# Optimization experiments

Hardware: AMD Instinct MI355X
Metric: run time of the kernel (lower is better)

## Reference

```python
import jax, jax.numpy as jnp
import numpy as np

NP_ = 20000   # paper nodes
NA_ = 20000   # author nodes
E_AP = 400000
E_PP = 400000
D_IN, D_H, HEADS, D_HEAD, D_FF, D_OUT = 128, 256, 8, 32, 2048, 64


def setup_inputs() -> dict:
    key = jax.random.key(0)
    ks = iter(jax.random.split(key, 48))
    def nrm(shape, s=0.1):
        return jax.random.normal(next(ks), shape, jnp.float32) * s
    inp = {
        'feat_paper': nrm((NP_, D_IN), 1.0),
        'feat_author': nrm((NA_, D_IN), 1.0),
        'W_in_p': nrm((D_H, D_IN)), 'b_in_p': nrm((D_H,), 0.05),
        'W_in_a': nrm((D_H, D_IN)), 'b_in_a': nrm((D_H,), 0.05),
        'W_gat_ap': nrm((D_H, D_H)), 'al_ap': nrm((HEADS, D_HEAD)), 'ar_ap': nrm((HEADS, D_HEAD)), 'b_gat_ap': nrm((D_H,), 0.05),
        'W_gat_pp': nrm((D_H, D_H)), 'al_pp': nrm((HEADS, D_HEAD)), 'ar_pp': nrm((HEADS, D_HEAD)), 'b_gat_pp': nrm((D_H,), 0.05),
        'Wqkv_s': nrm((3 * D_H, D_H)), 'bqkv_s': nrm((3 * D_H,), 0.05), 'Wo_s': nrm((D_H, D_H)), 'bo_s': nrm((D_H,), 0.05),
        'Wqkv_c': nrm((3 * D_H, D_H)), 'bqkv_c': nrm((3 * D_H,), 0.05), 'Wo_c': nrm((D_H, D_H)), 'bo_c': nrm((D_H,), 0.05),
        'W_ff1': nrm((D_FF, D_H)), 'b_ff1': nrm((D_FF,), 0.05),
        'W_ff2': nrm((D_H, D_FF)), 'b_ff2': nrm((D_H,), 0.05),
        'ln1_g': jnp.ones((D_H,), jnp.float32), 'ln1_b': jnp.zeros((D_H,), jnp.float32),
        'ln2_g': jnp.ones((D_H,), jnp.float32), 'ln2_b': jnp.zeros((D_H,), jnp.float32),
        'ln3_g': jnp.ones((D_H,), jnp.float32), 'ln3_b': jnp.zeros((D_H,), jnp.float32),
        'W_pred': nrm((D_OUT, 3 * D_H)), 'b_pred': nrm((D_OUT,), 0.05),
        'ap_src': jax.random.randint(next(ks), (E_AP,), 0, NA_),
        'ap_dst': jax.random.randint(next(ks), (E_AP,), 0, NP_),
        'pp_src': jax.random.randint(next(ks), (E_PP,), 0, NP_),
        'pp_dst': jax.random.randint(next(ks), (E_PP,), 0, NP_),
    }
    return inp


def _leaky(x):
    return jnp.where(x > 0, x, 0.2 * x)  # DGL GATConv negative_slope=0.2


def _gat(x, src, dst, W, al, ar, b):
    """DGL GATConv on homogeneous graph with self-loops appended (eval mode)."""
    N = x.shape[0]
    h = (x @ W.T).reshape(N, HEADS, D_HEAD)          # fc has no bias in GATConv
    el = (h * al[None]).sum(-1)                      # (N, H)
    er = (h * ar[None]).sum(-1)                      # (N, H)
    sl = jnp.arange(N, dtype=src.dtype)              # self loops (add_self_loop)
    s = jnp.concatenate([src, sl])
    d = jnp.concatenate([dst, sl])
    e = _leaky(el[s] + er[d])                        # (E+N, H)
    m = jax.ops.segment_max(e, d, num_segments=N)    # edge-softmax per dst
    a = jnp.exp(e - m[d])
    z = jax.ops.segment_sum(a, d, num_segments=N)
    out = jax.ops.segment_sum(a[:, :, None] * h[s], d, num_segments=N)
    out = out / z[:, :, None] + b.reshape(1, HEADS, D_HEAD)
    return out.reshape(N, D_H)                       # flatten(start_dim=1)


def _ln(x, g, b):
    mu = x.mean(-1, keepdims=True)
    v = ((x - mu) ** 2).mean(-1, keepdims=True)
    return (x - mu) / jnp.sqrt(v + 1e-5) * g + b


def _mha(xq, xkv, Wqkv, bqkv, Wo, bo):
    Wq, Wk, Wv = jnp.split(Wqkv, 3, axis=0)
    bq, bk, bv = jnp.split(bqkv, 3)
    B, S, _ = xq.shape
    Sk = xkv.shape[1]
    q = (xq @ Wq.T + bq).reshape(B, S, HEADS, D_HEAD)
    k = (xkv @ Wk.T + bk).reshape(B, Sk, HEADS, D_HEAD)
    v = (xkv @ Wv.T + bv).reshape(B, Sk, HEADS, D_HEAD)
    att = jnp.einsum('bqhd,bkhd->bhqk', q, k) * (D_HEAD ** -0.5)
    a = jax.nn.softmax(att, axis=-1)
    o = jnp.einsum('bhqk,bkhd->bqhd', a, v).reshape(B, S, D_H)
    return o @ Wo.T + bo


def reference(feat_paper, feat_author, W_in_p, b_in_p, W_in_a, b_in_a,
              W_gat_ap, al_ap, ar_ap, b_gat_ap, W_gat_pp, al_pp, ar_pp, b_gat_pp,
              Wqkv_s, bqkv_s, Wo_s, bo_s, Wqkv_c, bqkv_c, Wo_c, bo_c,
              W_ff1, b_ff1, W_ff2, b_ff2, ln1_g, ln1_b, ln2_g, ln2_b, ln3_g, ln3_b,
              W_pred, b_pred, ap_src, ap_dst, pp_src, pp_dst):
    # fc_in per node type
    hp = feat_paper @ W_in_p.T + b_in_p              # (NP, D_H)
    ha = feat_author @ W_in_a.T + b_in_a             # (NA, D_H)
    Na = ha.shape[0]
    # etype 'ap': bipartite author->paper, to_homogeneous orders [author; paper]
    x_ap = jnp.concatenate([ha, hp], axis=0)
    out_ap = _gat(x_ap, ap_src, ap_dst + Na, W_gat_ap, al_ap, ar_ap, b_gat_ap)[Na:]
    # etype 'pp': paper->paper (single node set)
    out_pp = _gat(hp, pp_src, pp_dst, W_gat_pp, al_pp, ar_pp, b_gat_pp)
    # h dict order: 'paper', 'paper-author', 'paper-paper'
    tgt = jnp.stack([hp, out_ap, out_pp], axis=1)    # (NP, 3, D_H)
    # TransformerDecoderLayer (post-norm, relu, eval): memory = tgt
    x = _ln(tgt + _mha(tgt, tgt, Wqkv_s, bqkv_s, Wo_s, bo_s), ln1_g, ln1_b)
    x = _ln(x + _mha(x, tgt, Wqkv_c, bqkv_c, Wo_c, bo_c), ln2_g, ln2_b)
    ff = jax.nn.relu(x @ W_ff1.T + b_ff1) @ W_ff2.T + b_ff2
    z = _ln(x + ff, ln3_g, ln3_b)
    return z.reshape(z.shape[0], -1) @ W_pred.T + b_pred
```

## Files before the change

kernel.cpp:

```cpp
#include <hip/hip_runtime.h>
#include <hip/hip_bf16.h>
#include <cstdint>
#include <cstddef>

#define NP_N 20000
#define NA_N 20000
#define E_AP_N 400000
#define E_PP_N 400000

typedef __attribute__((ext_vector_type(8))) short bf16x8;
typedef __attribute__((ext_vector_type(4))) float f32x4;

__device__ __forceinline__ float b2f(ushort u) { return __uint_as_float(((uint32_t)u) << 16); }
__device__ __forceinline__ ushort f2b(float f) {
    uint32_t x = __float_as_uint(f);
    return (ushort)((x + 0x7fffu + ((x >> 16) & 1u)) >> 16);
}

#define LGKM_BARRIER() do { \
    asm volatile("s_waitcnt lgkmcnt(0)" ::: "memory"); \
    __builtin_amdgcn_s_barrier(); \
    __builtin_amdgcn_sched_barrier(0); \
} while (0)

#define NJOBS 14
struct PackJobs {
    const float* src[NJOBS];
    void* dst[NJOBS];
    int M[NJOBS], K[NJOBS];
    int type[NJOBS];
    int nquad[NJOBS];
    int blk0[NJOBS];
};

__global__ void pack_all_kernel(PackJobs J)
{
    int b = blockIdx.x;
    int j = 0;
    while (j + 1 < NJOBS && b >= J.blk0[j + 1]) ++j;
    int u = (b - J.blk0[j]) * 256 + threadIdx.x;
    if (u >= J.nquad[j]) return;
    int ty = J.type[j];
    const float* src = J.src[j];
    if (ty == 3) {
        float4 v = ((const float4*)src)[u];
        ushort4 o;
        o.x = f2b(v.x); o.y = f2b(v.y); o.z = f2b(v.z); o.w = f2b(v.w);
        ((ushort4*)J.dst[j])[u] = o;
    } else if (ty == 4) {
        int4 z = {0, 0, 0, 0};
        ((int4*)J.dst[j])[u] = z;
    } else if (ty == 0) {
        int M = J.M[j], K = J.K[j];
        int KT = K >> 5;
        int q = u & 1023;
        int jt = u >> 10;
        int t = jt % KT, jj = jt / KT;
        int ks = q >> 8, rem = q & 255;
        int r = rem >> 1;
        int e0 = (rem & 1) * 4;
        int row = jj * 128 + r;
        ushort4 o = {0, 0, 0, 0};
        if (row < M) {
            const float* s = src + (size_t)row * K + t * 32 + ks * 8 + e0;
            o.x = f2b(s[0]); o.y = f2b(s[1]); o.z = f2b(s[2]); o.w = f2b(s[3]);
        }
        ((ushort4*)J.dst[j])[u] = o;
    } else if (ty == 1) {
        int q = u & 2047, chunk = u >> 11;
        int s = q >> 6, rem = q & 63;
        int fl = rem >> 1, e0 = (rem & 1) * 4;
        const float* sp = src + (size_t)(chunk * 32 + fl) * 256 + s * 8 + e0;
        ushort4 o;
        o.x = f2b(sp[0]); o.y = f2b(sp[1]); o.z = f2b(sp[2]); o.w = f2b(sp[3]);
        ((ushort4*)J.dst[j])[u] = o;
    } else {
        int q = u & 2047, chunk = u >> 11;
        int s2 = q >> 9, rem = q & 511;
        int c = rem >> 1, e0 = (rem & 1) * 4;
        const float* sp = src + (size_t)c * 2048 + chunk * 32 + s2 * 8 + e0;
        ushort4 o;
        o.x = f2b(sp[0]); o.y = f2b(sp[1]); o.z = f2b(sp[2]); o.w = f2b(sp[3]);
        ((ushort4*)J.dst[j])[u] = o;
    }
}

template <int OUT_MODE>
__global__ __launch_bounds__(256) void gemm_mfma(
    const ushort* __restrict__ A, const ushort* __restrict__ Bp,
    const float* __restrict__ bias, void* __restrict__ Cv,
    int N, int M, int K, int lda)
{
    __shared__ __align__(16) ushort Ab[3][4096];
    __shared__ __align__(16) ushort Bb[3][4096];
    const int tid = threadIdx.x;
    const int lane = tid & 63;
    const int w = tid >> 6;
    const int wr = w >> 1, wc = w & 1;
    const int row0 = blockIdx.x * 128;
    const int col0 = blockIdx.y * 128;
    const int KT = K >> 5;
    const ushort* Bbase = Bp + (size_t)blockIdx.y * KT * 4096;
    f32x4 acc[4][4] = {};

    size_t aoff[2];
#pragma unroll
    for (int i = 0; i < 2; ++i) {
        int r = row0 + i * 64 + lane;
        if (r > N - 1) r = N - 1;
        aoff[i] = (size_t)r * lda + w * 8;
    }

    auto stage = [&](int buf, int t) {
        const int k0 = t << 5;
#pragma unroll
        for (int i = 0; i < 2; ++i) {
            __builtin_amdgcn_global_load_lds(
                (const __attribute__((address_space(1))) void*)(A + aoff[i] + k0),
                (__attribute__((address_space(3))) void*)(&Ab[buf][(w * 2 + i) * 512]), 16, 0, 0);
        }
#pragma unroll
        for (int i = 0; i < 2; ++i) {
            __builtin_amdgcn_global_load_lds(
                (const __attribute__((address_space(1))) void*)(Bbase + (size_t)t * 4096 + (w * 2 + i) * 512 + lane * 8),
                (__attribute__((address_space(3))) void*)(&Bb[buf][(w * 2 + i) * 512]), 16, 0, 0);
        }
    };

    stage(0, 0);
    stage(1, 1);

    int cur = 0;
    for (int t = 0; t < KT; ++t) {
        if (t + 1 < KT) { asm volatile("s_waitcnt vmcnt(4)" ::: "memory"); }
        else            { asm volatile("s_waitcnt vmcnt(0)" ::: "memory"); }
        __builtin_amdgcn_s_barrier();
        __builtin_amdgcn_sched_barrier(0);
        if (t + 2 < KT) {
            int nb = cur - 1; if (nb < 0) nb = 2;
            stage(nb, t + 2);
        }

        bf16x8 af[4], bfr[4];
        const int ks = lane >> 4;
        const int rl = lane & 15;
#pragma unroll
        for (int m = 0; m < 4; ++m)
            af[m] = *(const bf16x8*)&Ab[cur][ks * 1024 + (wr * 64 + m * 16 + rl) * 8];
#pragma unroll
        for (int n = 0; n < 4; ++n)
            bfr[n] = *(const bf16x8*)&Bb[cur][ks * 1024 + (wc * 64 + n * 16 + rl) * 8];
#pragma unroll
        for (int m = 0; m < 4; ++m)
#pragma unroll
            for (int n = 0; n < 4; ++n)
                acc[m][n] = __builtin_amdgcn_mfma_f32_16x16x32_bf16(af[m], bfr[n], acc[m][n], 0, 0, 0);

        cur = (cur == 2) ? 0 : cur + 1;
    }

#pragma unroll
    for (int m = 0; m < 4; ++m) {
#pragma unroll
        for (int n = 0; n < 4; ++n) {
            int gc = col0 + wc * 64 + n * 16 + (lane & 15);
            if (gc >= M) continue;
            float bv = bias ? bias[gc] : 0.f;
#pragma unroll
            for (int r = 0; r < 4; ++r) {
                int grow = row0 + wr * 64 + m * 16 + (lane >> 4) * 4 + r;
                if (grow >= N) continue;
                float v = acc[m][n][r] + bv;
                if (OUT_MODE == 2) v = fmaxf(v, 0.f);
                if (OUT_MODE == 1) ((float*)Cv)[(size_t)grow * M + gc] = v;
                else ((ushort*)Cv)[(size_t)grow * M + gc] = f2b(v);
            }
        }
    }
}

static inline void gemm_bf(const ushort* A, const ushort* Bp, const float* bias, void* C,
                           int N, int M, int K, int lda, int mode, hipStream_t s)
{
    dim3 g((N + 127) / 128, (M + 127) / 128);
    if (mode == 0)      gemm_mfma<0><<<g, 256, 0, s>>>(A, Bp, bias, C, N, M, K, lda);
    else if (mode == 1) gemm_mfma<1><<<g, 256, 0, s>>>(A, Bp, bias, C, N, M, K, lda);
    else                gemm_mfma<2><<<g, 256, 0, s>>>(A, Bp, bias, C, N, M, K, lda);
}

__global__ __launch_bounds__(512) void ff_fused_kernel(
    const ushort* __restrict__ X, const ushort* __restrict__ W1p,
    const ushort* __restrict__ W2p, const float* __restrict__ b1,
    const float* __restrict__ b2, ushort* __restrict__ ffout, int N)
{
    __shared__ __align__(16) ushort W1buf[2][8192];
    __shared__ __align__(16) ushort W2buf[2][8192];
    __shared__ __align__(16) ushort Sbuf[4096];
    const int tid = threadIdx.x;
    const int lane = tid & 63;
    const int w = tid >> 6;
    const int wr = w >> 1, wc = w & 1;
    const int row0 = blockIdx.x * 128;
    const int rl = lane & 15;
    const int ks = lane >> 4;

    bf16x8 xf[2][8];
#pragma unroll
    for (int m = 0; m < 2; ++m) {
        int gr = row0 + wr * 32 + m * 16 + rl;
        if (gr > N - 1) gr = N - 1;
        const ushort* xrow = X + (size_t)gr * 256 + ks * 8;
#pragma unroll
        for (int kc = 0; kc < 8; ++kc)
            xf[m][kc] = *(const bf16x8*)(xrow + kc * 32);
    }

    f32x4 oacc[2][8] = {};

    auto stage = [&](int buf, int fc) {
#pragma unroll
        for (int i = 0; i < 4; ++i) {
            int ii = w * 4 + i;
            const ushort* src;
            ushort* dst;
            if (ii < 16) {
                src = W1p + (size_t)fc * 8192 + ii * 512 + lane * 8;
                dst = &W1buf[buf][ii * 512];
            } else {
                src = W2p + (size_t)fc * 8192 + (ii - 16) * 512 + lane * 8;
                dst = &W2buf[buf][(ii - 16) * 512];
            }
            __builtin_amdgcn_global_load_lds(
                (const __attribute__((address_space(1))) void*)src,
                (__attribute__((address_space(3))) void*)dst, 16, 0, 0);
        }
    };

    stage(0, 0);

    for (int fc = 0; fc < 64; ++fc) {
        const int cur = fc & 1;
        asm volatile("s_waitcnt vmcnt(0)" ::: "memory");
        __builtin_amdgcn_s_barrier();
        __builtin_amdgcn_sched_barrier(0);
        if (fc + 1 < 64) stage(cur ^ 1, fc + 1);

        f32x4 sacc[2] = {};
#pragma unroll
        for (int kc = 0; kc < 8; ++kc) {
            bf16x8 w1f = *(const bf16x8*)&W1buf[cur][(kc * 4 + ks) * 256 + (wc * 16 + rl) * 8];
#pragma unroll
            for (int m = 0; m < 2; ++m)
                sacc[m] = __builtin_amdgcn_mfma_f32_16x16x32_bf16(w1f, xf[m][kc], sacc[m], 0, 0, 0);
        }
        {
            const int f0 = fc * 32;
            const int fb = wc * 16 + ks * 4;
            const int sidx = wc * 2 + (ks >> 1);
            const int e0 = (ks & 1) * 4;
            float4 b1v = *(const float4*)&b1[f0 + fb];
#pragma unroll
            for (int m = 0; m < 2; ++m) {
                ushort4 o;
                o.x = f2b(fmaxf(sacc[m][0] + b1v.x, 0.f));
                o.y = f2b(fmaxf(sacc[m][1] + b1v.y, 0.f));
                o.z = f2b(fmaxf(sacc[m][2] + b1v.z, 0.f));
                o.w = f2b(fmaxf(sacc[m][3] + b1v.w, 0.f));
                *(ushort4*)&Sbuf[(sidx * 128 + wr * 32 + m * 16 + rl) * 8 + e0] = o;
            }
        }
        LGKM_BARRIER();

        {
            bf16x8 sf[2];
#pragma unroll
            for (int m = 0; m < 2; ++m)
                sf[m] = *(const bf16x8*)&Sbuf[(ks * 128 + wr * 32 + m * 16 + rl) * 8];
#pragma unroll
            for (int n = 0; n < 8; ++n) {
                bf16x8 w2f = *(const bf16x8*)&W2buf[cur][ks * 2048 + (wc * 128 + n * 16 + rl) * 8];
#pragma unroll
                for (int m = 0; m < 2; ++m)
                    oacc[m][n] = __builtin_amdgcn_mfma_f32_16x16x32_bf16(sf[m], w2f, oacc[m][n], 0, 0, 0);
            }
        }
    }

#pragma unroll
    for (int n = 0; n < 8; ++n) {
        int c = wc * 128 + n * 16 + rl;
        float bv = b2[c];
#pragma unroll
        for (int m = 0; m < 2; ++m) {
            int rbase = row0 + wr * 32 + m * 16 + ks * 4;
#pragma unroll
            for (int r = 0; r < 4; ++r) {
                int gr = rbase + r;
                if (gr < N) ffout[(size_t)gr * 256 + c] = f2b(oacc[m][n][r] + bv);
            }
        }
    }
}

__global__ void copy_col0_kernel(const ushort* __restrict__ src, ushort* __restrict__ tgt, int n)
{
    int i = blockIdx.x * blockDim.x + threadIdx.x;
    if (i >= n) return;
    int p = i >> 6, c = i & 63;
    ((ushort4*)tgt)[(size_t)p * 192 + c] = ((const ushort4*)src)[(size_t)p * 64 + c];
}

__global__ void attn_lr_all_kernel(
    const ushort* __restrict__ h0, const float* __restrict__ al0, const float* __restrict__ ar0,
    float* __restrict__ el0, float* __restrict__ er0,
    const ushort* __restrict__ h1, const float* __restrict__ al1, const float* __restrict__ ar1,
    float* __restrict__ el1, float* __restrict__ er1)
{
    int idx = blockIdx.x * blockDim.x + threadIdx.x;
    if (idx >= 480000) return;
    const ushort* h; const float *a1, *a2; float *el, *er; int i;
    if (idx < 320000) { h = h0; a1 = al0; a2 = ar0; el = el0; er = er0; i = idx; }
    else { h = h1; a1 = al1; a2 = ar1; el = el1; er = er1; i = idx - 320000; }
    int hd = i & 7;
    const ushort* hp = h + (size_t)(i >> 3) * 256 + hd * 32;
    const float* p1 = a1 + hd * 32;
    const float* p2 = a2 + hd * 32;
    float s1 = 0.f, s2 = 0.f;
#pragma unroll
    for (int j = 0; j < 8; ++j) {
        ushort4 t = ((const ushort4*)hp)[j];
        float v0 = b2f(t.x), v1 = b2f(t.y), v2 = b2f(t.z), v3 = b2f(t.w);
        s1 = fmaf(v0, p1[j * 4 + 0], s1); s2 = fmaf(v0, p2[j * 4 + 0], s2);
        s1 = fmaf(v1, p1[j * 4 + 1], s1); s2 = fmaf(v1, p2[j * 4 + 1], s2);
        s1 = fmaf(v2, p1[j * 4 + 2], s1); s2 = fmaf(v2, p2[j * 4 + 2], s2);
        s1 = fmaf(v3, p1[j * 4 + 3], s1); s2 = fmaf(v3, p2[j * 4 + 3], s2);
    }
    el[i] = s1;
    er[i] = s2;
}

__global__ void count2_kernel(const int* __restrict__ d0, int* __restrict__ c0,
                              const int* __restrict__ d1, int* __restrict__ c1, int E)
{
    int e = blockIdx.x * blockDim.x + threadIdx.x;
    if (e < E) atomicAdd(&c0[d0[e]], 1);
    else if (e < 2 * E) atomicAdd(&c1[d1[e - E]], 1);
}

__global__ void exscan2_kernel(int* __restrict__ deg0, int* __restrict__ offs0,
                               int* __restrict__ deg1, int* __restrict__ offs1, int N)
{
    int* deg = blockIdx.x ? deg1 : deg0;
    int* offs = blockIdx.x ? offs1 : offs0;
    __shared__ int sbuf[1024];
    __shared__ int carry;
    int tid = threadIdx.x;
    if (tid == 0) carry = 0;
    __syncthreads();
    for (int base = 0; base < N; base += 1024) {
        int i = base + tid;
        int v = (i < N) ? deg[i] : 0;
        sbuf[tid] = v;
        __syncthreads();
        for (int off = 1; off < 1024; off <<= 1) {
            int t = (tid >= off) ? sbuf[tid - off] : 0;
            __syncthreads();
            sbuf[tid] += t;
            __syncthreads();
        }
        if (i < N) offs[i] = carry + sbuf[tid] - v;
        int chunk_total = sbuf[1023];
        __syncthreads();
        if (tid == 0) carry += chunk_total;
        __syncthreads();
    }
    if (tid == 0) offs[N] = carry;
    __syncthreads();
    for (int i = tid; i < N; i += 1024) deg[i] = 0;
}

__global__ void scatter2_kernel(const int* __restrict__ s0, const int* __restrict__ d0,
                                const int* __restrict__ o0, int* __restrict__ c0, int* __restrict__ l0,
                                const int* __restrict__ s1, const int* __restrict__ d1,
                                const int* __restrict__ o1, int* __restrict__ c1, int* __restrict__ l1,
                                int E)
{
    int e = blockIdx.x * blockDim.x + threadIdx.x;
    if (e < E) {
        int d = d0[e];
        int pos = atomicAdd(&c0[d], 1);
        l0[o0[d] + pos] = s0[e];
    } else if (e < 2 * E) {
        int e1 = e - E;
        int d = d1[e1];
        int pos = atomicAdd(&c1[d], 1);
        l1[o1[d] + pos] = s1[e1];
    }
}

__global__ __launch_bounds__(64) void gat_agg_all_kernel(
    const ushort* __restrict__ ha, const float* __restrict__ ela, const float* __restrict__ era,
    const int* __restrict__ offsa, const int* __restrict__ lista, const float* __restrict__ biasa,
    const ushort* __restrict__ hp, const float* __restrict__ elp, const float* __restrict__ erp,
    const int* __restrict__ offsp, const int* __restrict__ listp, const float* __restrict__ biasp,
    ushort* __restrict__ out)
{
    int bid = blockIdx.x;
    const ushort* h; const float *el, *er, *bias; const int *offs, *elist;
    int p, dn, coloff;
    if (bid < NP_N) {
        h = ha; el = ela; er = era; offs = offsa; elist = lista; bias = biasa;
        p = bid; dn = NA_N + p; coloff = 256;
    } else {
        h = hp; el = elp; er = erp; offs = offsp; elist = listp; bias = biasp;
        p = bid - NP_N; dn = p; coloff = 512;
    }
    int l = threadIdx.x;
    int head = l >> 3;
    float erv = er[(size_t)dn * 8 + head];
    float acc[4] = {0.f, 0.f, 0.f, 0.f};
    float z = 0.f;
    int beg = offs[p], end = offs[p + 1];
    for (int e = beg - 1; e < end; ++e) {
        int s = (e < beg) ? dn : elist[e];
        float x = el[(size_t)s * 8 + head] + erv;
        x = x > 0.f ? x : 0.2f * x;
        float wgt = expf(x);
        z += wgt;
        ushort4 hv = *(const ushort4*)&h[(size_t)s * 256 + l * 4];
        acc[0] = fmaf(wgt, b2f(hv.x), acc[0]);
        acc[1] = fmaf(wgt, b2f(hv.y), acc[1]);
        acc[2] = fmaf(wgt, b2f(hv.z), acc[2]);
        acc[3] = fmaf(wgt, b2f(hv.w), acc[3]);
    }
    float inv = 1.f / z;
    ushort4 o;
    o.x = f2b(acc[0] * inv + bias[l * 4 + 0]);
    o.y = f2b(acc[1] * inv + bias[l * 4 + 1]);
    o.z = f2b(acc[2] * inv + bias[l * 4 + 2]);
    o.w = f2b(acc[3] * inv + bias[l * 4 + 3]);
    *(ushort4*)&out[(size_t)p * 768 + coloff + l * 4] = o;
}

__global__ void mha3_kernel(const ushort* qb, int ldq, int qoff,
                            const ushort* kvb, int ldkv, int koff, int voff,
                            ushort* ob, int ldo, int NPn)
{
    int idx = blockIdx.x * blockDim.x + threadIdx.x;
    if (idx >= NPn * 24) return;
    int h = idx & 7;
    int i = (idx >> 3) % 3;
    int p = idx / 24;
    float qr[32];
    {
        const ushort* q = qb + (size_t)(p * 3 + i) * ldq + qoff + h * 32;
#pragma unroll
        for (int j = 0; j < 8; ++j) {
            ushort4 t = ((const ushort4*)q)[j];
            qr[j * 4 + 0] = b2f(t.x); qr[j * 4 + 1] = b2f(t.y);
            qr[j * 4 + 2] = b2f(t.z); qr[j * 4 + 3] = b2f(t.w);
        }
    }
    float s[3];
#pragma unroll
    for (int j = 0; j < 3; ++j) {
        const ushort* k = kvb + (size_t)(p * 3 + j) * ldkv + koff + h * 32;
        float a = 0.f;
#pragma unroll
        for (int t4 = 0; t4 < 8; ++t4) {
            ushort4 t = ((const ushort4*)k)[t4];
            a = fmaf(qr[t4 * 4 + 0], b2f(t.x), a);
            a = fmaf(qr[t4 * 4 + 1], b2f(t.y), a);
            a = fmaf(qr[t4 * 4 + 2], b2f(t.z), a);
            a = fmaf(qr[t4 * 4 + 3], b2f(t.w), a);
        }
        s[j] = a * 0.17677669529663687f;
    }
    float m = fmaxf(s[0], fmaxf(s[1], s[2]));
    float e0 = expf(s[0] - m), e1 = expf(s[1] - m), e2 = expf(s[2] - m);
    float inv = 1.f / (e0 + e1 + e2);
    float aw[3] = {e0 * inv, e1 * inv, e2 * inv};
    float o[32] = {};
#pragma unroll
    for (int j = 0; j < 3; ++j) {
        const ushort* v = kvb + (size_t)(p * 3 + j) * ldkv + voff + h * 32;
#pragma unroll
        for (int t4 = 0; t4 < 8; ++t4) {
            ushort4 t = ((const ushort4*)v)[t4];
            o[t4 * 4 + 0] = fmaf(aw[j], b2f(t.x), o[t4 * 4 + 0]);
            o[t4 * 4 + 1] = fmaf(aw[j], b2f(t.y), o[t4 * 4 + 1]);
            o[t4 * 4 + 2] = fmaf(aw[j], b2f(t.z), o[t4 * 4 + 2]);
            o[t4 * 4 + 3] = fmaf(aw[j], b2f(t.w), o[t4 * 4 + 3]);
        }
    }
    ushort* op = ob + (size_t)(p * 3 + i) * ldo + h * 32;
#pragma unroll
    for (int t4 = 0; t4 < 8; ++t4) {
        ushort4 t;
        t.x = f2b(o[t4 * 4 + 0]); t.y = f2b(o[t4 * 4 + 1]);
        t.z = f2b(o[t4 * 4 + 2]); t.w = f2b(o[t4 * 4 + 3]);
        ((ushort4*)op)[t4] = t;
    }
}

__global__ __launch_bounds__(256) void add_ln_kernel(
    const ushort* __restrict__ a, const ushort* __restrict__ b,
    const float* __restrict__ g, const float* __restrict__ be,
    ushort* __restrict__ out, int rows)
{
    int row = blockIdx.x * 4 + (threadIdx.x >> 6);
    if (row >= rows) return;
    int l = threadIdx.x & 63;
    ushort4 va = *(const ushort4*)&a[(size_t)row * 256 + l * 4];
    ushort4 vb = *(const ushort4*)&b[(size_t)row * 256 + l * 4];
    float v[4];
    v[0] = b2f(va.x) + b2f(vb.x);
    v[1] = b2f(va.y) + b2f(vb.y);
    v[2] = b2f(va.z) + b2f(vb.z);
    v[3] = b2f(va.w) + b2f(vb.w);
    float s = v[0] + v[1] + v[2] + v[3];
#pragma unroll
    for (int off = 32; off; off >>= 1) s += __shfl_xor(s, off);
    float mean = s * (1.f / 256.f);
    float s2 = 0.f;
#pragma unroll
    for (int j = 0; j < 4; ++j) { float d = v[j] - mean; s2 = fmaf(d, d, s2); }
#pragma unroll
    for (int off = 32; off; off >>= 1) s2 += __shfl_xor(s2, off);
    float rstd = rsqrtf(s2 * (1.f / 256.f) + 1e-5f);
    ushort4 o;
    o.x = f2b((v[0] - mean) * rstd * g[l * 4 + 0] + be[l * 4 + 0]);
    o.y = f2b((v[1] - mean) * rstd * g[l * 4 + 1] + be[l * 4 + 1]);
    o.z = f2b((v[2] - mean) * rstd * g[l * 4 + 2] + be[l * 4 + 2]);
    o.w = f2b((v[3] - mean) * rstd * g[l * 4 + 3] + be[l * 4 + 3]);
    *(ushort4*)&out[(size_t)row * 256 + l * 4] = o;
}

extern "C" void kernel_launch(void* const* d_in, const int* in_sizes, int n_in,
                              void* d_out, int out_size, void* d_ws, size_t ws_size,
                              hipStream_t stream)
{
    const float* feat_paper  = (const float*)d_in[0];
    const float* feat_author = (const float*)d_in[1];
    const float* W_in_p  = (const float*)d_in[2];
    const float* b_in_p  = (const float*)d_in[3];
    const float* W_in_a  = (const float*)d_in[4];
    const float* b_in_a  = (const float*)d_in[5];
    const float* W_gat_ap = (const float*)d_in[6];
    const float* al_ap    = (const float*)d_in[7];
    const float* ar_ap    = (const float*)d_in[8];
    const float* b_gat_ap = (const float*)d_in[9];
    const float* W_gat_pp = (const float*)d_in[10];
    const float* al_pp    = (const float*)d_in[11];
    const float* ar_pp    = (const float*)d_in[12];
    const float* b_gat_pp = (const float*)d_in[13];
    const float* Wqkv_s = (const float*)d_in[14];
    const float* bqkv_s = (const float*)d_in[15];
    const float* Wo_s   = (const float*)d_in[16];
    const float* bo_s   = (const float*)d_in[17];
    const float* Wqkv_c = (const float*)d_in[18];
    const float* bqkv_c = (const float*)d_in[19];
    const float* Wo_c   = (const float*)d_in[20];
    const float* bo_c   = (const float*)d_in[21];
    const float* W_ff1  = (const float*)d_in[22];
    const float* b_ff1  = (const float*)d_in[23];
    const float* W_ff2  = (const float*)d_in[24];
    const float* b_ff2  = (const float*)d_in[25];
    const float* ln1_g  = (const float*)d_in[26];
    const float* ln1_b  = (const float*)d_in[27];
    const float* ln2_g  = (const float*)d_in[28];
    const float* ln2_b  = (const float*)d_in[29];
    const float* ln3_g  = (const float*)d_in[30];
    const float* ln3_b  = (const float*)d_in[31];
    const float* W_pred = (const float*)d_in[32];
    const float* b_pred = (const float*)d_in[33];
    const int* ap_src = (const int*)d_in[34];
    const int* ap_dst = (const int*)d_in[35];
    const int* pp_src = (const int*)d_in[36];
    const int* pp_dst = (const int*)d_in[37];

    const int NP = NP_N, NA = NA_N;

    uint8_t* wsb = (uint8_t*)d_ws;
    ushort* tgt_bf = (ushort*)wsb;
    ushort* X_bf   = (ushort*)(wsb + 30720000);
    ushort* WB     = (ushort*)(wsb + 61440000);
    ushort* p_in_p   = WB + 0;
    ushort* p_in_a   = WB + 32768;
    ushort* p_gat_ap = WB + 65536;
    ushort* p_gat_pp = WB + 131072;
    ushort* p_qkv_s  = WB + 196608;
    ushort* p_o_s    = WB + 393216;
    ushort* p_qkv_c  = WB + 458752;
    ushort* p_o_c    = WB + 655360;
    ushort* p_pred   = WB + 720896;
    ushort* p_ff1    = WB + 819200;
    ushort* p_ff2    = WB + 1343488;
    uint8_t* BIG = wsb + 65280000;

    ushort* feat_p_bf = (ushort*)BIG;
    ushort* feat_a_bf = (ushort*)(BIG + 5120000);
    ushort* x_ap_bf   = (ushort*)(BIG + 10240000);
    ushort* hp_bf     = x_ap_bf + (size_t)NA * 256;
    ushort* h_ap_bf   = (ushort*)(BIG + 30720000);
    ushort* h_pp_bf   = (ushort*)(BIG + 51200000);
    float* el_ap = (float*)(BIG + 61440000);
    float* er_ap = (float*)(BIG + 62720000);
    float* el_pp = (float*)(BIG + 64000000);
    float* er_pp = (float*)(BIG + 64640000);
    int* ireg    = (int*)(BIG + 65280000);
    int* ap_offs = ireg;
    int* pp_offs = ireg + 20004;
    int* ap_cur  = ireg + 40008;
    int* pp_cur  = ireg + 60008;
    int* ap_list = ireg + 80008;
    int* pp_list = ireg + 480008;

    {
        PackJobs J;
        const float* srcs[NJOBS] = { feat_paper, feat_author, W_in_p, W_in_a, W_gat_ap,
                                     W_gat_pp, Wqkv_s, Wo_s, Wqkv_c, Wo_c, W_pred,
                                     W_ff1, W_ff2, nullptr };
        void* dsts[NJOBS] = { feat_p_bf, feat_a_bf, p_in_p, p_in_a, p_gat_ap,
                              p_gat_pp, p_qkv_s, p_o_s, p_qkv_c, p_o_c, p_pred,
                              p_ff1, p_ff2, ap_cur };
        int Ms[NJOBS]  = {0,0, 256,256,256,256, 768,256,768,256, 64, 0,0, 0};
        int Ks[NJOBS]  = {0,0, 128,128,256,256, 256,256,256,256, 768, 0,0, 0};
        int tys[NJOBS] = {3,3, 0,0,0,0, 0,0,0,0, 0, 1,2, 4};
        int nq[NJOBS]  = {640000,640000, 8192,8192,16384,16384, 49152,16384,49152,16384,
                          24576, 131072,131072, 10000};
        int acc = 0;
        for (int j = 0; j < NJOBS; ++j) {
            J.src[j] = srcs[j]; J.dst[j] = dsts[j];
            J.M[j] = Ms[j]; J.K[j] = Ks[j]; J.type[j] = tys[j]; J.nquad[j] = nq[j];
            J.blk0[j] = acc;
            acc += (nq[j] + 255) / 256;
        }
        pack_all_kernel<<<acc, 256, 0, stream>>>(J);
    }

    gemm_bf(feat_a_bf, p_in_a, b_in_a, x_ap_bf, NA, 256, 128, 128, 0, stream);
    gemm_bf(feat_p_bf, p_in_p, b_in_p, hp_bf,   NP, 256, 128, 128, 0, stream);

    copy_col0_kernel<<<(NP * 64 + 255) / 256, 256, 0, stream>>>(hp_bf, tgt_bf, NP * 64);

    gemm_bf(x_ap_bf, p_gat_ap, nullptr, h_ap_bf, NA + NP, 256, 256, 256, 0, stream);
    gemm_bf(hp_bf,   p_gat_pp, nullptr, h_pp_bf, NP,      256, 256, 256, 0, stream);

    attn_lr_all_kernel<<<1875, 256, 0, stream>>>(h_ap_bf, al_ap, ar_ap, el_ap, er_ap,
                                                 h_pp_bf, al_pp, ar_pp, el_pp, er_pp);

    count2_kernel<<<3125, 256, 0, stream>>>(ap_dst, ap_cur, pp_dst, pp_cur, E_AP_N);
    exscan2_kernel<<<2, 1024, 0, stream>>>(ap_cur, ap_offs, pp_cur, pp_offs, NP);
    scatter2_kernel<<<3125, 256, 0, stream>>>(ap_src, ap_dst, ap_offs, ap_cur, ap_list,
                                              pp_src, pp_dst, pp_offs, pp_cur, pp_list, E_AP_N);

    gat_agg_all_kernel<<<2 * NP, 64, 0, stream>>>(
        h_ap_bf, el_ap, er_ap, ap_offs, ap_list, b_gat_ap,
        h_pp_bf, el_pp, er_pp, pp_offs, pp_list, b_gat_pp, tgt_bf);

    {
        ushort* qkv = (ushort*)BIG;
        gemm_bf(tgt_bf, p_qkv_s, bqkv_s, qkv, 60000, 768, 256, 256, 0, stream);
        mha3_kernel<<<(NP * 24 + 255) / 256, 256, 0, stream>>>(qkv, 768, 0, qkv, 768, 256, 512, qkv, 768, NP);
        gemm_bf(qkv, p_o_s, bo_s, X_bf, 60000, 256, 256, 768, 0, stream);
        add_ln_kernel<<<15000, 256, 0, stream>>>(tgt_bf, X_bf, ln1_g, ln1_b, X_bf, 60000);
    }

    {
        ushort* qb  = (ushort*)BIG;
        ushort* kvb = (ushort*)(BIG + 30720000);
        const ushort* p_kv_c = p_qkv_c + (size_t)2 * 8 * 4096;
        gemm_bf(X_bf,   p_qkv_c, bqkv_c,       qb,  60000, 256, 256, 256, 0, stream);
        gemm_bf(tgt_bf, p_kv_c,  bqkv_c + 256, kvb, 60000, 512, 256, 256, 0, stream);
        mha3_kernel<<<(NP * 24 + 255) / 256, 256, 0, stream>>>(qb, 256, 0, kvb, 512, 0, 256, qb, 256, NP);
        gemm_bf(qb, p_o_c, bo_c, kvb, 60000, 256, 256, 256, 0, stream);
        add_ln_kernel<<<15000, 256, 0, stream>>>(X_bf, kvb, ln2_g, ln2_b, X_bf, 60000);
    }

    {
        ushort* ffo = (ushort*)BIG;
        ff_fused_kernel<<<(60000 + 127) / 128, 512, 0, stream>>>(X_bf, p_ff1, p_ff2, b_ff1, b_ff2, ffo, 60000);
        add_ln_kernel<<<15000, 256, 0, stream>>>(X_bf, ffo, ln3_g, ln3_b, X_bf, 60000);
    }

    gemm_bf(X_bf, p_pred, b_pred, (float*)d_out, NP, 64, 768, 768, 1, stream);
}
```

Baseline: 869.3 us.

## Fuse FFN with residual LayerNorm, shrink FF tiles, parallelize degree scan

```diff
diff --git a/kernel.cpp b/kernel.cpp
--- a/kernel.cpp
+++ b/kernel.cpp
@@ -188,19 +188,20 @@
     else                gemm_mfma<2><<<g, 256, 0, s>>>(A, Bp, bias, C, N, M, K, lda);
 }
 
-__global__ __launch_bounds__(512) void ff_fused_kernel(
-    const ushort* __restrict__ X, const ushort* __restrict__ W1p,
-    const ushort* __restrict__ W2p, const float* __restrict__ b1,
-    const float* __restrict__ b2, ushort* __restrict__ ffout, int N)
+__global__ __launch_bounds__(256, 2) void ff_ln_kernel(
+    const ushort* __restrict__ W1p, const ushort* __restrict__ W2p,
+    const float* __restrict__ b1, const float* __restrict__ b2,
+    const float* __restrict__ g3, const float* __restrict__ be3,
+    ushort* X, int N)
 {
     __shared__ __align__(16) ushort W1buf[2][8192];
     __shared__ __align__(16) ushort W2buf[2][8192];
-    __shared__ __align__(16) ushort Sbuf[4096];
+    __shared__ __align__(16) ushort Sbuf[2048];
     const int tid = threadIdx.x;
     const int lane = tid & 63;
     const int w = tid >> 6;
     const int wr = w >> 1, wc = w & 1;
-    const int row0 = blockIdx.x * 128;
+    const int row0 = blockIdx.x * 64;
     const int rl = lane & 15;
     const int ks = lane >> 4;
 
@@ -219,8 +220,8 @@
 
     auto stage = [&](int buf, int fc) {
 #pragma unroll
-        for (int i = 0; i < 4; ++i) {
-            int ii = w * 4 + i;
+        for (int i = 0; i < 8; ++i) {
+            int ii = w * 8 + i;
             const ushort* src;
             ushort* dst;
             if (ii < 16) {
@@ -266,7 +267,7 @@
                 o.y = f2b(fmaxf(sacc[m][1] + b1v.y, 0.f));
                 o.z = f2b(fmaxf(sacc[m][2] + b1v.z, 0.f));
                 o.w = f2b(fmaxf(sacc[m][3] + b1v.w, 0.f));
-                *(ushort4*)&Sbuf[(sidx * 128 + wr * 32 + m * 16 + rl) * 8 + e0] = o;
+                *(ushort4*)&Sbuf[(sidx * 64 + wr * 32 + m * 16 + rl) * 8 + e0] = o;
             }
         }
         LGKM_BARRIER();
@@ -275,7 +276,7 @@
             bf16x8 sf[2];
 #pragma unroll
             for (int m = 0; m < 2; ++m)
-                sf[m] = *(const bf16x8*)&Sbuf[(ks * 128 + wr * 32 + m * 16 + rl) * 8];
+                sf[m] = *(const bf16x8*)&Sbuf[ks * 512 + (wr * 32 + m * 16 + rl) * 8];
 #pragma unroll
             for (int n = 0; n < 8; ++n) {
                 bf16x8 w2f = *(const bf16x8*)&W2buf[cur][ks * 2048 + (wc * 128 + n * 16 + rl) * 8];
@@ -284,21 +285,70 @@
                     oacc[m][n] = __builtin_amdgcn_mfma_f32_16x16x32_bf16(sf[m], w2f, oacc[m][n], 0, 0, 0);
             }
         }
-    }
-
+        __syncthreads();
+    }
+
+    float2* lnb = (float2*)W1buf;
+    float psum[2][4] = {}, psq[2][4] = {};
 #pragma unroll
     for (int n = 0; n < 8; ++n) {
         int c = wc * 128 + n * 16 + rl;
         float bv = b2[c];
 #pragma unroll
-        for (int m = 0; m < 2; ++m) {
-            int rbase = row0 + wr * 32 + m * 16 + ks * 4;
+        for (int m = 0; m < 2; ++m)
 #pragma unroll
             for (int r = 0; r < 4; ++r) {
-                int gr = rbase + r;
-                if (gr < N) ffout[(size_t)gr * 256 + c] = f2b(oacc[m][n][r] + bv);
+                int grow = row0 + wr * 32 + m * 16 + ks * 4 + r;
+                float v = oacc[m][n][r] + bv + b2f(X[(size_t)grow * 256 + c]);
+                oacc[m][n][r] = v;
+                psum[m][r] += v;
+                psq[m][r] = fmaf(v, v, psq[m][r]);
             }
-        }
+    }
+#pragma unroll
+    for (int off = 8; off >= 1; off >>= 1)
+#pragma unroll
+        for (int m = 0; m < 2; ++m)
+#pragma unroll
+            for (int r = 0; r < 4; ++r) {
+                psum[m][r] += __shfl_xor(psum[m][r], off);
+                psq[m][r]  += __shfl_xor(psq[m][r], off);
+            }
+    if (rl == 0) {
+#pragma unroll
+        for (int m = 0; m < 2; ++m)
+#pragma unroll
+            for (int r = 0; r < 4; ++r) {
+                int lr = wr * 32 + m * 16 + ks * 4 + r;
+                lnb[wc * 64 + lr] = make_float2(psum[m][r], psq[m][r]);
+            }
+    }
+    __syncthreads();
+    float mean_[2][4], rstd_[2][4];
+#pragma unroll
+    for (int m = 0; m < 2; ++m)
+#pragma unroll
+        for (int r = 0; r < 4; ++r) {
+            int lr = wr * 32 + m * 16 + ks * 4 + r;
+            float2 a0 = lnb[lr], a1 = lnb[64 + lr];
+            float mean = (a0.x + a1.x) * (1.f / 256.f);
+            float var = (a0.y + a1.y) * (1.f / 256.f) - mean * mean;
+            mean_[m][r] = mean;
+            rstd_[m][r] = rsqrtf(var + 1e-5f);
+        }
+#pragma unroll
+    for (int n = 0; n < 8; ++n) {
+        int c = wc * 128 + n * 16 + rl;
+        float gv = g3[c], bev = be3[c];
+#pragma unroll
+        for (int m = 0; m < 2; ++m)
+#pragma unroll
+            for (int r = 0; r < 4; ++r) {
+                int grow = row0 + wr * 32 + m * 16 + ks * 4 + r;
+                if (grow < N)
+                    X[(size_t)grow * 256 + c] =
+                        f2b((oacc[m][n][r] - mean_[m][r]) * rstd_[m][r] * gv + bev);
+            }
     }
 }
 
@@ -347,36 +397,52 @@
     else if (e < 2 * E) atomicAdd(&c1[d1[e - E]], 1);
 }
 
-__global__ void exscan2_kernel(int* __restrict__ deg0, int* __restrict__ offs0,
-                               int* __restrict__ deg1, int* __restrict__ offs1, int N)
-{
-    int* deg = blockIdx.x ? deg1 : deg0;
-    int* offs = blockIdx.x ? offs1 : offs0;
+__global__ void scan_chunk_kernel(const int* __restrict__ deg0, int* __restrict__ offs0,
+                                  const int* __restrict__ deg1, int* __restrict__ offs1,
+                                  int* __restrict__ parts, int N)
+{
+    int es = blockIdx.x / 20, ch = blockIdx.x % 20;
+    const int* deg = es ? deg1 : deg0;
+    int* offs = es ? offs1 : offs0;
     __shared__ int sbuf[1024];
-    __shared__ int carry;
     int tid = threadIdx.x;
-    if (tid == 0) carry = 0;
+    int i = ch * 1024 + tid;
+    int v = (i < N) ? deg[i] : 0;
+    sbuf[tid] = v;
     __syncthreads();
-    for (int base = 0; base < N; base += 1024) {
-        int i = base + tid;
-        int v = (i < N) ? deg[i] : 0;
-        sbuf[tid] = v;
+    for (int off = 1; off < 1024; off <<= 1) {
+        int t = (tid >= off) ? sbuf[tid - off] : 0;
         __syncthreads();
-        for (int off = 1; off < 1024; off <<= 1) {
-            int t = (tid >= off) ? sbuf[tid - off] : 0;
-            __syncthreads();
-            sbuf[tid] += t;
-            __syncthreads();
-        }
-        if (i < N) offs[i] = carry + sbuf[tid] - v;
-        int chunk_total = sbuf[1023];
+        sbuf[tid] += t;
         __syncthreads();
-        if (tid == 0) carry += chunk_total;
-        __syncthreads();
-    }
-    if (tid == 0) offs[N] = carry;
-    __syncthreads();
-    for (int i = tid; i < N; i += 1024) deg[i] = 0;
+    }
+    if (i < N) offs[i] = sbuf[tid] - v;
+    if (tid == 1023) parts[es * 21 + ch] = sbuf[1023];
+}
+
+__global__ void scan_parts_kernel(int* __restrict__ parts)
+{
+    int t = threadIdx.x;
+    if ((t & 31) == 0 && t < 64) {
+        int* p = parts + (t >> 5) * 21;
+        int acc = 0;
+#pragma unroll
+        for (int i = 0; i < 20; ++i) { int x = p[i]; p[i] = acc; acc += x; }
+        p[20] = acc;
+    }
+}
+
+__global__ void scan_final_kernel(int* __restrict__ deg0, int* __restrict__ offs0,
+                                  int* __restrict__ deg1, int* __restrict__ offs1,
+                                  const int* __restrict__ parts, int N)
+{
+    int es = blockIdx.x / 20, ch = blockIdx.x % 20;
+    int* deg = es ? deg1 : deg0;
+    int* offs = es ? offs1 : offs0;
+    int tid = threadIdx.x;
+    int i = ch * 1024 + tid;
+    if (i < N) { offs[i] += parts[es * 21 + ch]; deg[i] = 0; }
+    if (ch == 19 && tid == 1023) offs[N] = parts[es * 21 + 20];
 }
 
 __global__ void scatter2_kernel(const int* __restrict__ s0, const int* __restrict__ d0,
@@ -615,6 +681,7 @@
     int* pp_cur  = ireg + 60008;
     int* ap_list = ireg + 80008;
     int* pp_list = ireg + 480008;
+    int* parts   = ireg + 880008;
 
     {
         PackJobs J;
@@ -651,7 +718,9 @@
                                                  h_pp_bf, al_pp, ar_pp, el_pp, er_pp);
 
     count2_kernel<<<3125, 256, 0, stream>>>(ap_dst, ap_cur, pp_dst, pp_cur, E_AP_N);
-    exscan2_kernel<<<2, 1024, 0, stream>>>(ap_cur, ap_offs, pp_cur, pp_offs, NP);
+    scan_chunk_kernel<<<40, 1024, 0, stream>>>(ap_cur, ap_offs, pp_cur, pp_offs, parts, NP);
+    scan_parts_kernel<<<1, 64, 0, stream>>>(parts);
+    scan_final_kernel<<<40, 1024, 0, stream>>>(ap_cur, ap_offs, pp_cur, pp_offs, parts, NP);
     scatter2_kernel<<<3125, 256, 0, stream>>>(ap_src, ap_dst, ap_offs, ap_cur, ap_list,
                                               pp_src, pp_dst, pp_offs, pp_cur, pp_list, E_AP_N);
 
@@ -678,11 +747,8 @@
         add_ln_kernel<<<15000, 256, 0, stream>>>(X_bf, kvb, ln2_g, ln2_b, X_bf, 60000);
     }
 
-    {
-        ushort* ffo = (ushort*)BIG;
-        ff_fused_kernel<<<(60000 + 127) / 128, 512, 0, stream>>>(X_bf, p_ff1, p_ff2, b_ff1, b_ff2, ffo, 60000);
-        add_ln_kernel<<<15000, 256, 0, stream>>>(X_bf, ffo, ln3_g, ln3_b, X_bf, 60000);
-    }
+    ff_ln_kernel<<<(60000 + 63) / 64, 256, 0, stream>>>(p_ff1, p_ff2, b_ff1, b_ff2,
+                                                        ln3_g, ln3_b, X_bf, 60000);
 
     gemm_bf(X_bf, p_pred, b_pred, (float*)d_out, NP, 64, 768, 768, 1, stream);
 }
```

Measured after the change: 825.1 us. 1.05x faster.
